# Optimization experiments

Measured on AMD Instinct MI355X. Metric: run time of the kernel, lower is better.

The kernel has to match this reference:

```python
import jax, jax.numpy as jnp
import numpy as np

T, B, C, N, H = 4, 32, 384, 196, 12
D = C // H
HID = 1536
ALPHA = 4.0  # spikingjelly default sigmoid surrogate alpha
EPS = 1e-5   # BatchNorm eps
SCALE = 0.25

@jax.custom_vjp
def spike(x):
    return (x >= 0.0).astype(x.dtype)

def _spike_fwd(x):
    return (x >= 0.0).astype(x.dtype), x

def _spike_bwd(x, g):
    s = jax.nn.sigmoid(ALPHA * x)
    return (g * ALPHA * s * (1.0 - s),)

spike.defvjp(_spike_fwd, _spike_bwd)

def lif(x, thr=1.0, tau=2.0):
    # Multi-step LIF, hard reset to 0, detach_reset=True; x: (T, ...)
    def step(v, xt):
        v = v + (xt - v) / tau
        s = spike(v - thr)
        v = v * (1.0 - jax.lax.stop_gradient(s))
        return v, s
    _, out = jax.lax.scan(step, jnp.zeros_like(x[0]), x)
    return out

def conv_bn(x, w, b, g, beta, m, var):
    # 1x1 Conv1d (= channel matmul) + inference-form BatchNorm1d; x: (T,B,Cin,N), w: (Cout,Cin)
    y = jnp.einsum('tbcn,oc->tbon', x, w)
    if b is not None:
        y = y + b[:, None]
    inv = g * jax.lax.rsqrt(var + EPS)
    return y * inv[:, None] + (beta - m * inv)[:, None]

def _heads(t):
    # (T,B,C,N) -> (T,B,H,N,D), matching transpose(-1,-2).reshape(T,B,N,H,D).permute(0,1,3,2,4)
    return jnp.swapaxes(t, -1, -2).reshape(T, B, N, H, D).transpose(0, 1, 3, 2, 4)

def block_fwd(x, policy, wq, qg, qb, qm, qv, wk, kg, kb, km, kvv, wv, vg, vb, vm, vvv,
              wp, bp, pg, pb, pm, pv, w1, b1, g1, be1, m1, v1, w2, b2, g2, be2, m2, v2):
    q = _heads(lif(conv_bn(x, wq, None, qg, qb, qm, qv)))
    k = _heads(lif(conv_bn(x, wk, None, kg, kb, km, kvv)))
    v = _heads(lif(conv_bn(x, wv, None, vg, vb, vm, vvv)))
    attn = jnp.einsum('tbhnd,tbhmd->tbhnm', q, k)           # (T,B,H,N,N)
    pr = policy.reshape(T, B, 1, 1, N)
    eye = jnp.eye(N, dtype=x.dtype)
    attn = attn * (pr + (1.0 - pr) * eye)                   # attention_policy masking
    o = jnp.einsum('tbhnm,tbhmd->tbhnd', attn, v) * SCALE
    o = jnp.swapaxes(o, 3, 4).reshape(T, B, C, N)           # transpose(3,4).reshape(T,B,C,N)
    o = lif(o, thr=0.5)                                     # attn_lif v_threshold=0.5
    o = lif(conv_bn(o, wp, bp, pg, pb, pm, pv))             # proj conv+bn+lif
    x = x + o                                               # residual 1
    h = lif(conv_bn(x, w1, b1, g1, be1, m1, v1))            # MLP fc1
    h = lif(conv_bn(h, w2, b2, g2, be2, m2, v2))            # MLP fc2
    return x + h                                            # residual 2

def setup_inputs():
    key = jax.random.key(0)
    ks = iter(jax.random.split(key, 48))
    def nrm(shape, s=1.0):
        return jax.random.normal(next(ks), shape, jnp.float32) * s
    def uni(shape):
        return jax.random.uniform(next(ks), shape, jnp.float32, minval=0.5, maxval=1.5)
    inp = {}
    inp['x'] = nrm((T, B, C, N))
    inp['policy'] = (jax.random.uniform(next(ks), (T * B, N, 1)) > 0.3).astype(jnp.float32)
    inp.update({'wq': nrm((C, C), 0.05), 'qg': jnp.ones((C,)), 'qb': jnp.zeros((C,)), 'qm': nrm((C,), 0.1), 'qv': uni((C,))})
    inp.update({'wk': nrm((C, C), 0.05), 'kg': jnp.ones((C,)), 'kb': jnp.zeros((C,)), 'km': nrm((C,), 0.1), 'kvv': uni((C,))})
    inp.update({'wv': nrm((C, C), 0.05), 'vg': jnp.ones((C,)), 'vb': jnp.zeros((C,)), 'vm': nrm((C,), 0.1), 'vvv': uni((C,))})
    inp.update({'wp': nrm((C, C), 0.05), 'bp': jnp.zeros((C,)), 'pg': jnp.ones((C,)), 'pb': jnp.zeros((C,)), 'pm': nrm((C,), 0.1), 'pv': uni((C,))})
    inp.update({'w1': nrm((HID, C), 0.05), 'b1': jnp.zeros((HID,)), 'g1': jnp.ones((HID,)), 'be1': jnp.zeros((HID,)), 'm1': nrm((HID,), 0.1), 'v1': uni((HID,))})
    inp.update({'w2': nrm((C, HID), 0.05), 'b2': jnp.zeros((C,)), 'g2': jnp.ones((C,)), 'be2': jnp.zeros((C,)), 'm2': nrm((C,), 0.1), 'v2': uni((C,))})
    return inp

def reference(x, policy, wq, qg, qb, qm, qv, wk, kg, kb, km, kvv, wv, vg, vb, vm, vvv,
              wp, bp, pg, pb, pm, pv, w1, b1, g1, be1, m1, v1, w2, b2, g2, be2, m2, v2):
    return block_fwd(x, policy, wq, qg, qb, qm, qv, wk, kg, kb, km, kvv, wv, vg, vb, vm, vvv,
                     wp, bp, pg, pb, pm, pv, w1, b1, g1, be1, m1, v1, w2, b2, g2, be2, m2, v2)
```

## Files before the change

kernel.cpp:

```cpp
#include <hip/hip_runtime.h>
#include <cstdint>
#include <cstddef>

#define N_POS 196

__device__ __forceinline__ void async_copy16(const float* g, float* l) {
    __builtin_amdgcn_global_load_lds(
        (const __attribute__((address_space(1))) uint32_t*)g,
        (__attribute__((address_space(3))) uint32_t*)l,
        16, 0, 0);
}

template<int CIN, bool USE_FMA, bool ACCUM>
__global__ __launch_bounds__(512) void convbn_kernel(
    const float* __restrict__ X, const float* __restrict__ W,
    const float* __restrict__ Bi, const float* __restrict__ Ga,
    const float* __restrict__ Be, const float* __restrict__ Mu,
    const float* __restrict__ Va, float* __restrict__ Y, int Cout,
    int nb, int b0, int xlocal, int ylocal)
{
    constexpr int NCH = CIN / 16;
    __shared__ float lds[2 * 3136 + 2 * 1024];
    float* Xs = lds;
    float* Ws = lds + 6272;
    const int tid = threadIdx.x;
    const int l   = blockIdx.x;
    const int t   = l / nb;
    const int bl  = l - t * nb;
    const int tbg = t * 32 + b0 + bl;
    const int xtb = xlocal ? l : tbg;
    const int ytb = ylocal ? l : tbg;
    const int o0  = blockIdx.y * 64;
    const int n0  = tid & 63;
    const int obase = (tid >> 6) * 8;
    const int col3 = (n0 < 4) ? (n0 + 192) : 196;
    const float* Xtb = X + (size_t)xtb * CIN * N_POS;
    const float* Wp  = W + (size_t)o0 * CIN;

    float acc[8][4];
    #pragma unroll
    for (int i = 0; i < 8; ++i)
        #pragma unroll
        for (int j = 0; j < 4; ++j) acc[i][j] = 0.f;

    auto stage = [&](int buf, int kc) {
        const int oo = tid >> 3, k2 = (tid & 7) * 2;
        float2 wv2 = *(const float2*)(Wp + (size_t)oo * CIN + kc + k2);
        {
            int i = tid;
            const float* g = Xtb + (size_t)(kc + i / 49) * N_POS + (i % 49) * 4;
            async_copy16(g, &Xs[buf * 3136 + (i & ~63) * 4]);
        }
        if (tid < 272) {
            int i = tid + 512;
            const float* g = Xtb + (size_t)(kc + i / 49) * N_POS + (i % 49) * 4;
            async_copy16(g, &Xs[buf * 3136 + (i & ~63) * 4]);
        }
        Ws[buf * 1024 + k2 * 64 + oo]       = wv2.x;
        Ws[buf * 1024 + (k2 + 1) * 64 + oo] = wv2.y;
    };

    stage(0, 0);
    __syncthreads();

    int buf = 0;
    for (int ch = 0; ch < NCH; ++ch) {
        if (ch + 1 < NCH) stage(buf ^ 1, (ch + 1) * 16);
        const float* Xb = Xs + buf * 3136;
        const float* Wb = Ws + buf * 1024;
        #pragma unroll 4
        for (int kk = 0; kk < 16; ++kk) {
            float4 wA = *(const float4*)(Wb + kk * 64 + obase);
            float4 wB = *(const float4*)(Wb + kk * 64 + obase + 4);
            float xv[4] = { Xb[kk * 196 + n0], Xb[kk * 196 + n0 + 64],
                            Xb[kk * 196 + n0 + 128], Xb[kk * 196 + col3] };
            float wv[8] = { wA.x, wA.y, wA.z, wA.w, wB.x, wB.y, wB.z, wB.w };
            #pragma unroll
            for (int i = 0; i < 8; ++i)
                #pragma unroll
                for (int j = 0; j < 4; ++j) {
                    if (USE_FMA) acc[i][j] = fmaf(wv[i], xv[j], acc[i][j]);
                    else         acc[i][j] = __fadd_rn(acc[i][j], __fmul_rn(wv[i], xv[j]));
                }
        }
        __syncthreads();
        buf ^= 1;
    }

    #pragma unroll
    for (int i = 0; i < 8; ++i) {
        int o = o0 + obase + i;
        float sc = __fmul_rn(Ga[o], 1.0f / sqrtf(__fadd_rn(Va[o], 1e-5f)));
        float sh = __fsub_rn(Be[o], __fmul_rn(Mu[o], sc));
        float* yp = Y + ((size_t)ytb * Cout + o) * N_POS;
        #pragma unroll
        for (int j = 0; j < 4; ++j) {
            if (j == 3 && n0 >= 4) continue;
            float y = acc[i][j];
            if (Bi) y = __fadd_rn(y, Bi[o]);
            float r = __fadd_rn(__fmul_rn(y, sc), sh);
            int n = n0 + j * 64;
            if (ACCUM) yp[n] = __fadd_rn(yp[n], r);
            else       yp[n] = r;
        }
    }
}

__global__ __launch_bounds__(256) void lif_kernel(float* __restrict__ Y, int plane4, float thr)
{
    int idx = blockIdx.x * 256 + threadIdx.x;
    if (idx >= plane4) return;
    float4* Yp = (float4*)Y;
    float v0 = 0.f, v1 = 0.f, v2 = 0.f, v3 = 0.f;
    #pragma unroll
    for (int t = 0; t < 4; ++t) {
        float4 xv = Yp[(size_t)t * plane4 + idx];
        v0 = __fadd_rn(v0, __fmul_rn(__fsub_rn(xv.x, v0), 0.5f));
        v1 = __fadd_rn(v1, __fmul_rn(__fsub_rn(xv.y, v1), 0.5f));
        v2 = __fadd_rn(v2, __fmul_rn(__fsub_rn(xv.z, v2), 0.5f));
        v3 = __fadd_rn(v3, __fmul_rn(__fsub_rn(xv.w, v3), 0.5f));
        float s0 = (__fsub_rn(v0, thr) >= 0.f) ? 1.f : 0.f;
        float s1 = (__fsub_rn(v1, thr) >= 0.f) ? 1.f : 0.f;
        float s2 = (__fsub_rn(v2, thr) >= 0.f) ? 1.f : 0.f;
        float s3 = (__fsub_rn(v3, thr) >= 0.f) ? 1.f : 0.f;
        v0 = __fmul_rn(v0, 1.f - s0); v1 = __fmul_rn(v1, 1.f - s1);
        v2 = __fmul_rn(v2, 1.f - s2); v3 = __fmul_rn(v3, 1.f - s3);
        xv.x = s0; xv.y = s1; xv.z = s2; xv.w = s3;
        Yp[(size_t)t * plane4 + idx] = xv;
    }
}

__global__ __launch_bounds__(256) void lif_add_kernel(
    const float* __restrict__ Yin, float* __restrict__ Out, int b0)
{
    const int PL4 = 8 * 384 * 49;
    const int B4  = 384 * 49;
    int idx = blockIdx.x * 256 + threadIdx.x;
    if (idx >= PL4) return;
    int bl = idx / B4, r = idx - bl * B4;
    const float4* Yp = (const float4*)Yin;
    float v0 = 0.f, v1 = 0.f, v2 = 0.f, v3 = 0.f;
    #pragma unroll
    for (int t = 0; t < 4; ++t) {
        float4 xv = Yp[(size_t)t * PL4 + idx];
        v0 = __fadd_rn(v0, __fmul_rn(__fsub_rn(xv.x, v0), 0.5f));
        v1 = __fadd_rn(v1, __fmul_rn(__fsub_rn(xv.y, v1), 0.5f));
        v2 = __fadd_rn(v2, __fmul_rn(__fsub_rn(xv.z, v2), 0.5f));
        v3 = __fadd_rn(v3, __fmul_rn(__fsub_rn(xv.w, v3), 0.5f));
        float s0 = (__fsub_rn(v0, 1.0f) >= 0.f) ? 1.f : 0.f;
        float s1 = (__fsub_rn(v1, 1.0f) >= 0.f) ? 1.f : 0.f;
        float s2 = (__fsub_rn(v2, 1.0f) >= 0.f) ? 1.f : 0.f;
        float s3 = (__fsub_rn(v3, 1.0f) >= 0.f) ? 1.f : 0.f;
        v0 = __fmul_rn(v0, 1.f - s0); v1 = __fmul_rn(v1, 1.f - s1);
        v2 = __fmul_rn(v2, 1.f - s2); v3 = __fmul_rn(v3, 1.f - s3);
        float4* op = (float4*)Out + ((size_t)(t * 32 + b0 + bl) * B4 + r);
        float4 o = *op;
        o.x = __fadd_rn(o.x, s0); o.y = __fadd_rn(o.y, s1);
        o.z = __fadd_rn(o.z, s2); o.w = __fadd_rn(o.w, s3);
        *op = o;
    }
}

__global__ __launch_bounds__(256) void pack_kernel(const float* __restrict__ S,
                                                   uint32_t* __restrict__ Bits)
{
    int idx = blockIdx.x * 256 + threadIdx.x;
    if (idx >= 4 * 32 * 12 * 196) return;
    int n = idx % 196;
    int rest = idx / 196;
    int h = rest % 12;
    int tb = rest / 12;
    const float* sp = S + ((size_t)tb * 384 + h * 32) * 196 + n;
    uint32_t bits = 0;
    #pragma unroll
    for (int d = 0; d < 32; ++d)
        bits |= (sp[(size_t)d * 196] > 0.5f) ? (1u << d) : 0u;
    Bits[idx] = bits;
}

__global__ __launch_bounds__(256) void attn_kernel(
    const uint32_t* __restrict__ Qb, const uint32_t* __restrict__ Kb,
    const float* __restrict__ V, const float* __restrict__ P, float* __restrict__ O)
{
    __shared__ uint32_t Qbs[196], Kbs[196];
    __shared__ float Ps[196];
    __shared__ float Vs[32][204];
    __shared__ float Ss[32][204];
    __shared__ float Os[32][36];
    const int tid = threadIdx.x;
    const int bid = blockIdx.x;
    const int tb = bid / 12, h = bid - tb * 12;
    const size_t vbase = ((size_t)tb * 384 + h * 32) * 196;
    const size_t qbase = ((size_t)tb * 12 + h) * 196;
    for (int i = tid; i < 196; i += 256) {
        Qbs[i] = Qb[qbase + i];
        Kbs[i] = Kb[qbase + i];
        Ps[i]  = P[(size_t)tb * 196 + i];
    }
    for (int i = tid; i < 32 * 49; i += 256) {
        int d = i / 49, m4 = i - d * 49;
        *(float4*)&Vs[d][m4 * 4] = *(const float4*)(V + vbase + (size_t)d * 196 + m4 * 4);
    }
    __syncthreads();
    for (int n0 = 0; n0 < 196; n0 += 32) {
        const int rows = min(32, 196 - n0);
        for (int idx = tid; idx < rows * 196; idx += 256) {
            int ns = idx / 196, m = idx - ns * 196;
            int n = n0 + ns;
            float s = (float)__popc(Qbs[n] & Kbs[m]);
            float p = Ps[m];
            float e = (m == n) ? 1.f : 0.f;
            Ss[ns][m] = s * (p + (1.f - p) * e);
        }
        __syncthreads();
        {
            const int tn = tid & 15, td = tid >> 4;
            float a00 = 0, a01 = 0, a10 = 0, a11 = 0;
            #pragma unroll 7
            for (int m4 = 0; m4 < 49; ++m4) {
                float4 s0 = *(const float4*)&Ss[tn][m4 * 4];
                float4 s1 = *(const float4*)&Ss[tn + 16][m4 * 4];
                float4 u0 = *(const float4*)&Vs[td][m4 * 4];
                float4 u1 = *(const float4*)&Vs[td + 16][m4 * 4];
                a00 += s0.x * u0.x + s0.y * u0.y + s0.z * u0.z + s0.w * u0.w;
                a01 += s0.x * u1.x + s0.y * u1.y + s0.z * u1.z + s0.w * u1.w;
                a10 += s1.x * u0.x + s1.y * u0.y + s1.z * u0.z + s1.w * u0.w;
                a11 += s1.x * u1.x + s1.y * u1.y + s1.z * u1.z + s1.w * u1.w;
            }
            Os[td     ][tn     ] = a00 * 0.25f;
            Os[td + 16][tn     ] = a01 * 0.25f;
            Os[td     ][tn + 16] = a10 * 0.25f;
            Os[td + 16][tn + 16] = a11 * 0.25f;
        }
        __syncthreads();
        {
            const int d = tid >> 3, c4 = tid & 7;
            if (c4 * 4 < rows)
                *(float4*)(O + vbase + (size_t)d * 196 + n0 + c4 * 4) =
                    *(const float4*)&Os[d][c4 * 4];
        }
        __syncthreads();
    }
}

__global__ __launch_bounds__(256) void add_kernel(const float* __restrict__ A,
    const float* __restrict__ B, float* __restrict__ Out, int n4)
{
    int idx = blockIdx.x * 256 + threadIdx.x;
    if (idx >= n4) return;
    float4 a = ((const float4*)A)[idx];
    float4 b = ((const float4*)B)[idx];
    float4 o;
    o.x = __fadd_rn(a.x, b.x); o.y = __fadd_rn(a.y, b.y);
    o.z = __fadd_rn(a.z, b.z); o.w = __fadd_rn(a.w, b.w);
    ((float4*)Out)[idx] = o;
}

extern "C" void kernel_launch(void* const* d_in, const int* in_sizes, int n_in,
                              void* d_out, int out_size, void* d_ws, size_t ws_size,
                              hipStream_t stream) {
    const float* x   = (const float*)d_in[0];
    const float* pol = (const float*)d_in[1];
    const float* wq = (const float*)d_in[2];
    const float* qg = (const float*)d_in[3];
    const float* qb = (const float*)d_in[4];
    const float* qm = (const float*)d_in[5];
    const float* qv = (const float*)d_in[6];
    const float* wk = (const float*)d_in[7];
    const float* kg = (const float*)d_in[8];
    const float* kb = (const float*)d_in[9];
    const float* km = (const float*)d_in[10];
    const float* kvv= (const float*)d_in[11];
    const float* wv = (const float*)d_in[12];
    const float* vg = (const float*)d_in[13];
    const float* vb = (const float*)d_in[14];
    const float* vm = (const float*)d_in[15];
    const float* vvv= (const float*)d_in[16];
    const float* wp = (const float*)d_in[17];
    const float* bp = (const float*)d_in[18];
    const float* pg = (const float*)d_in[19];
    const float* pb = (const float*)d_in[20];
    const float* pm = (const float*)d_in[21];
    const float* pv = (const float*)d_in[22];
    const float* w1 = (const float*)d_in[23];
    const float* b1 = (const float*)d_in[24];
    const float* g1 = (const float*)d_in[25];
    const float* be1= (const float*)d_in[26];
    const float* m1 = (const float*)d_in[27];
    const float* v1 = (const float*)d_in[28];
    const float* w2 = (const float*)d_in[29];
    const float* b2 = (const float*)d_in[30];
    const float* g2 = (const float*)d_in[31];
    const float* be2= (const float*)d_in[32];
    const float* m2 = (const float*)d_in[33];
    const float* v2 = (const float*)d_in[34];

    float* bufA = (float*)d_ws;
    float* bufD = bufA + 9633792;
    uint32_t* Qbits = (uint32_t*)(bufD + 2408448);
    uint32_t* Kbits = Qbits + 301056;
    float* out = (float*)d_out;

    convbn_kernel<384, false, false><<<dim3(128, 6), 512, 0, stream>>>(x, wq, nullptr, qg, qb, qm, qv, bufA, 384, 32, 0, 0, 0);
    lif_kernel<<<2352, 256, 0, stream>>>(bufA, 602112, 1.0f);
    pack_kernel<<<1176, 256, 0, stream>>>(bufA, Qbits);
    convbn_kernel<384, false, false><<<dim3(128, 6), 512, 0, stream>>>(x, wk, nullptr, kg, kb, km, kvv, bufA, 384, 32, 0, 0, 0);
    lif_kernel<<<2352, 256, 0, stream>>>(bufA, 602112, 1.0f);
    pack_kernel<<<1176, 256, 0, stream>>>(bufA, Kbits);
    convbn_kernel<384, false, false><<<dim3(128, 6), 512, 0, stream>>>(x, wv, nullptr, vg, vb, vm, vvv, bufA, 384, 32, 0, 0, 0);
    lif_kernel<<<2352, 256, 0, stream>>>(bufA, 602112, 1.0f);

    attn_kernel<<<1536, 256, 0, stream>>>(Qbits, Kbits, bufA, pol, out);
    lif_kernel<<<2352, 256, 0, stream>>>(out, 602112, 0.5f);

    convbn_kernel<384, true, false><<<dim3(128, 6), 512, 0, stream>>>(out, wp, bp, pg, pb, pm, pv, bufA, 384, 32, 0, 0, 0);
    lif_kernel<<<2352, 256, 0, stream>>>(bufA, 602112, 1.0f);
    add_kernel<<<9408, 256, 0, stream>>>(x, bufA, out, 2408448);

    for (int c = 0; c < 4; ++c) {
        convbn_kernel<384, false, false><<<dim3(32, 24), 512, 0, stream>>>(out, w1, b1, g1, be1, m1, v1, bufA, 1536, 8, c * 8, 0, 1);
        lif_kernel<<<2352, 256, 0, stream>>>(bufA, 602112, 1.0f);
        convbn_kernel<1536, true, false><<<dim3(32, 6), 512, 0, stream>>>(bufA, w2, b2, g2, be2, m2, v2, bufD, 384, 8, c * 8, 1, 1);
        lif_add_kernel<<<588, 256, 0, stream>>>(bufD, out, c * 8);
    }
}
```

Before: 2.249 ms.

## Pre-transpose conv weights and read wave-uniform weights directly instead of via LDS

Adds a transpose kernel that lays each 1x1 conv weight matrix out as (Cin, Cout) in workspace at the start of every call. The convbn kernel then drops its LDS staging of weights and reads eight contiguous per-wave-uniform weights straight from global memory, which the compiler can turn into scalar loads. Each lane now owns four consecutive positions as a float4, with vectorized float4 stores, and 15 of the 64 lanes per wave sit idle. The trade-offs are six extra small launches per call, the wasted lanes, and reliance on cache for repeated weight reads.

```diff
diff --git a/kernel.cpp b/kernel.cpp
--- a/kernel.cpp
+++ b/kernel.cpp
@@ -3,6 +3,8 @@
 #include <cstddef>
 
 #define N_POS 196
+
+typedef __attribute__((ext_vector_type(4))) float f32x4;
 
 __device__ __forceinline__ void async_copy16(const float* g, float* l) {
     __builtin_amdgcn_global_load_lds(
@@ -11,18 +13,37 @@
         16, 0, 0);
 }
 
+__global__ __launch_bounds__(256) void transpose_kernel(
+    const float* __restrict__ A, float* __restrict__ At, int R, int C)
+{
+    __shared__ float tile[32][33];
+    const int c0 = blockIdx.x * 32, r0 = blockIdx.y * 32;
+    const int tx = threadIdx.x & 31, ty = threadIdx.x >> 5;
+    #pragma unroll
+    for (int dy = 0; dy < 32; dy += 8) {
+        int r = r0 + ty + dy, c = c0 + tx;
+        if (r < R && c < C) tile[ty + dy][tx] = A[(size_t)r * C + c];
+    }
+    __syncthreads();
+    #pragma unroll
+    for (int dy = 0; dy < 32; dy += 8) {
+        int c = c0 + ty + dy, r = r0 + tx;
+        if (c < C && r < R) At[(size_t)c * R + r] = tile[tx][ty + dy];
+    }
+}
+
 template<int CIN, bool USE_FMA, bool ACCUM>
 __global__ __launch_bounds__(512) void convbn_kernel(
-    const float* __restrict__ X, const float* __restrict__ W,
+    const float* __restrict__ X, const float* __restrict__ Wt,
     const float* __restrict__ Bi, const float* __restrict__ Ga,
     const float* __restrict__ Be, const float* __restrict__ Mu,
     const float* __restrict__ Va, float* __restrict__ Y, int Cout,
     int nb, int b0, int xlocal, int ylocal)
 {
+#pragma clang fp contract(off)
     constexpr int NCH = CIN / 16;
-    __shared__ float lds[2 * 3136 + 2 * 1024];
-    float* Xs = lds;
-    float* Ws = lds + 6272;
+    __shared__ f32x4 XsV[2 * 784];
+    float* Xs = (float*)XsV;
     const int tid = threadIdx.x;
     const int l   = blockIdx.x;
     const int t   = l / nb;
@@ -31,57 +52,47 @@
     const int xtb = xlocal ? l : tbg;
     const int ytb = ylocal ? l : tbg;
     const int o0  = blockIdx.y * 64;
-    const int n0  = tid & 63;
-    const int obase = (tid >> 6) * 8;
-    const int col3 = (n0 < 4) ? (n0 + 192) : 196;
+    const int lane = tid & 63;
+    const int ob  = __builtin_amdgcn_readfirstlane((tid >> 6) * 8);
+    const int q4  = (lane < 49) ? lane : 48;
+    const bool alive = (lane < 49);
     const float* Xtb = X + (size_t)xtb * CIN * N_POS;
-    const float* Wp  = W + (size_t)o0 * CIN;
-
-    float acc[8][4];
-    #pragma unroll
-    for (int i = 0; i < 8; ++i)
-        #pragma unroll
-        for (int j = 0; j < 4; ++j) acc[i][j] = 0.f;
+
+    f32x4 acc[8];
+    #pragma unroll
+    for (int i = 0; i < 8; ++i) acc[i] = (f32x4)0.f;
 
     auto stage = [&](int buf, int kc) {
-        const int oo = tid >> 3, k2 = (tid & 7) * 2;
-        float2 wv2 = *(const float2*)(Wp + (size_t)oo * CIN + kc + k2);
-        {
-            int i = tid;
-            const float* g = Xtb + (size_t)(kc + i / 49) * N_POS + (i % 49) * 4;
-            async_copy16(g, &Xs[buf * 3136 + (i & ~63) * 4]);
-        }
+        int i = tid;
+        async_copy16(Xtb + (size_t)(kc + i / 49) * N_POS + (i % 49) * 4,
+                     &Xs[buf * 3136 + (i & ~63) * 4]);
         if (tid < 272) {
-            int i = tid + 512;
-            const float* g = Xtb + (size_t)(kc + i / 49) * N_POS + (i % 49) * 4;
-            async_copy16(g, &Xs[buf * 3136 + (i & ~63) * 4]);
-        }
-        Ws[buf * 1024 + k2 * 64 + oo]       = wv2.x;
-        Ws[buf * 1024 + (k2 + 1) * 64 + oo] = wv2.y;
+            i = tid + 512;
+            async_copy16(Xtb + (size_t)(kc + i / 49) * N_POS + (i % 49) * 4,
+                         &Xs[buf * 3136 + (i & ~63) * 4]);
+        }
     };
 
     stage(0, 0);
     __syncthreads();
-
     int buf = 0;
     for (int ch = 0; ch < NCH; ++ch) {
         if (ch + 1 < NCH) stage(buf ^ 1, (ch + 1) * 16);
         const float* Xb = Xs + buf * 3136;
-        const float* Wb = Ws + buf * 1024;
-        #pragma unroll 4
+        const float* Wk = Wt + (size_t)(ch * 16) * Cout + o0 + ob;
+        #pragma unroll 8
         for (int kk = 0; kk < 16; ++kk) {
-            float4 wA = *(const float4*)(Wb + kk * 64 + obase);
-            float4 wB = *(const float4*)(Wb + kk * 64 + obase + 4);
-            float xv[4] = { Xb[kk * 196 + n0], Xb[kk * 196 + n0 + 64],
-                            Xb[kk * 196 + n0 + 128], Xb[kk * 196 + col3] };
-            float wv[8] = { wA.x, wA.y, wA.z, wA.w, wB.x, wB.y, wB.z, wB.w };
+            f32x4 xq = *(const f32x4*)(Xb + kk * 196 + q4 * 4);
+            const float* wr = Wk + (size_t)kk * Cout;
+            float w8[8];
             #pragma unroll
-            for (int i = 0; i < 8; ++i)
-                #pragma unroll
-                for (int j = 0; j < 4; ++j) {
-                    if (USE_FMA) acc[i][j] = fmaf(wv[i], xv[j], acc[i][j]);
-                    else         acc[i][j] = __fadd_rn(acc[i][j], __fmul_rn(wv[i], xv[j]));
-                }
+            for (int i = 0; i < 8; ++i) w8[i] = wr[i];
+            #pragma unroll
+            for (int i = 0; i < 8; ++i) {
+                f32x4 wd = { w8[i], w8[i], w8[i], w8[i] };
+                if (USE_FMA) acc[i] = __builtin_elementwise_fma(wd, xq, acc[i]);
+                else         acc[i] = acc[i] + wd * xq;
+            }
         }
         __syncthreads();
         buf ^= 1;
@@ -89,20 +100,28 @@
 
     #pragma unroll
     for (int i = 0; i < 8; ++i) {
-        int o = o0 + obase + i;
+        int o = o0 + ob + i;
         float sc = __fmul_rn(Ga[o], 1.0f / sqrtf(__fadd_rn(Va[o], 1e-5f)));
         float sh = __fsub_rn(Be[o], __fmul_rn(Mu[o], sc));
-        float* yp = Y + ((size_t)ytb * Cout + o) * N_POS;
-        #pragma unroll
-        for (int j = 0; j < 4; ++j) {
-            if (j == 3 && n0 >= 4) continue;
-            float y = acc[i][j];
-            if (Bi) y = __fadd_rn(y, Bi[o]);
-            float r = __fadd_rn(__fmul_rn(y, sc), sh);
-            int n = n0 + j * 64;
-            if (ACCUM) yp[n] = __fadd_rn(yp[n], r);
-            else       yp[n] = r;
-        }
+        if (!alive) continue;
+        float* yp = Y + ((size_t)ytb * Cout + o) * N_POS + q4 * 4;
+        float r0_ = acc[i].x, r1_ = acc[i].y, r2_ = acc[i].z, r3_ = acc[i].w;
+        if (Bi) {
+            float b = Bi[o];
+            r0_ = __fadd_rn(r0_, b); r1_ = __fadd_rn(r1_, b);
+            r2_ = __fadd_rn(r2_, b); r3_ = __fadd_rn(r3_, b);
+        }
+        float4 r;
+        r.x = __fadd_rn(__fmul_rn(r0_, sc), sh);
+        r.y = __fadd_rn(__fmul_rn(r1_, sc), sh);
+        r.z = __fadd_rn(__fmul_rn(r2_, sc), sh);
+        r.w = __fadd_rn(__fmul_rn(r3_, sc), sh);
+        if (ACCUM) {
+            float4 y = *(const float4*)yp;
+            r.x = __fadd_rn(y.x, r.x); r.y = __fadd_rn(y.y, r.y);
+            r.z = __fadd_rn(y.z, r.z); r.w = __fadd_rn(y.w, r.w);
+        }
+        *(float4*)yp = r;
     }
 }
 
@@ -299,28 +318,41 @@
     float* bufD = bufA + 9633792;
     uint32_t* Qbits = (uint32_t*)(bufD + 2408448);
     uint32_t* Kbits = Qbits + 301056;
+    float* wqT = (float*)(Kbits + 301056);
+    float* wkT = wqT + 147456;
+    float* wvT = wkT + 147456;
+    float* wpT = wvT + 147456;
+    float* w1T = wpT + 147456;
+    float* w2T = w1T + 589824;
     float* out = (float*)d_out;
 
-    convbn_kernel<384, false, false><<<dim3(128, 6), 512, 0, stream>>>(x, wq, nullptr, qg, qb, qm, qv, bufA, 384, 32, 0, 0, 0);
+    transpose_kernel<<<dim3(12, 12), 256, 0, stream>>>(wq, wqT, 384, 384);
+    transpose_kernel<<<dim3(12, 12), 256, 0, stream>>>(wk, wkT, 384, 384);
+    transpose_kernel<<<dim3(12, 12), 256, 0, stream>>>(wv, wvT, 384, 384);
+    transpose_kernel<<<dim3(12, 12), 256, 0, stream>>>(wp, wpT, 384, 384);
+    transpose_kernel<<<dim3(12, 48), 256, 0, stream>>>(w1, w1T, 1536, 384);
+    transpose_kernel<<<dim3(48, 12), 256, 0, stream>>>(w2, w2T, 384, 1536);
+
+    convbn_kernel<384, false, false><<<dim3(128, 6), 512, 0, stream>>>(x, wqT, nullptr, qg, qb, qm, qv, bufA, 384, 32, 0, 0, 0);
     lif_kernel<<<2352, 256, 0, stream>>>(bufA, 602112, 1.0f);
     pack_kernel<<<1176, 256, 0, stream>>>(bufA, Qbits);
-    convbn_kernel<384, false, false><<<dim3(128, 6), 512, 0, stream>>>(x, wk, nullptr, kg, kb, km, kvv, bufA, 384, 32, 0, 0, 0);
+    convbn_kernel<384, false, false><<<dim3(128, 6), 512, 0, stream>>>(x, wkT, nullptr, kg, kb, km, kvv, bufA, 384, 32, 0, 0, 0);
     lif_kernel<<<2352, 256, 0, stream>>>(bufA, 602112, 1.0f);
     pack_kernel<<<1176, 256, 0, stream>>>(bufA, Kbits);
-    convbn_kernel<384, false, false><<<dim3(128, 6), 512, 0, stream>>>(x, wv, nullptr, vg, vb, vm, vvv, bufA, 384, 32, 0, 0, 0);
+    convbn_kernel<384, false, false><<<dim3(128, 6), 512, 0, stream>>>(x, wvT, nullptr, vg, vb, vm, vvv, bufA, 384, 32, 0, 0, 0);
     lif_kernel<<<2352, 256, 0, stream>>>(bufA, 602112, 1.0f);
 
     attn_kernel<<<1536, 256, 0, stream>>>(Qbits, Kbits, bufA, pol, out);
     lif_kernel<<<2352, 256, 0, stream>>>(out, 602112, 0.5f);
 
-    convbn_kernel<384, true, false><<<dim3(128, 6), 512, 0, stream>>>(out, wp, bp, pg, pb, pm, pv, bufA, 384, 32, 0, 0, 0);
+    convbn_kernel<384, true, false><<<dim3(128, 6), 512, 0, stream>>>(out, wpT, bp, pg, pb, pm, pv, bufA, 384, 32, 0, 0, 0);
     lif_kernel<<<2352, 256, 0, stream>>>(bufA, 602112, 1.0f);
     add_kernel<<<9408, 256, 0, stream>>>(x, bufA, out, 2408448);
 
     for (int c = 0; c < 4; ++c) {
-        convbn_kernel<384, false, false><<<dim3(32, 24), 512, 0, stream>>>(out, w1, b1, g1, be1, m1, v1, bufA, 1536, 8, c * 8, 0, 1);
+        convbn_kernel<384, false, false><<<dim3(32, 24), 512, 0, stream>>>(out, w1T, b1, g1, be1, m1, v1, bufA, 1536, 8, c * 8, 0, 1);
         lif_kernel<<<2352, 256, 0, stream>>>(bufA, 602112, 1.0f);
-        convbn_kernel<1536, true, false><<<dim3(32, 6), 512, 0, stream>>>(bufA, w2, b2, g2, be2, m2, v2, bufD, 384, 8, c * 8, 1, 1);
+        convbn_kernel<1536, true, false><<<dim3(32, 6), 512, 0, stream>>>(bufA, w2T, b2, g2, be2, m2, v2, bufD, 384, 8, c * 8, 1, 1);
         lif_add_kernel<<<588, 256, 0, stream>>>(bufD, out, c * 8);
     }
 }
```

Result: slower. 3.449 ms (+53.3%).
